# Kernel optimization log

Hardware: AMD Instinct MI355X
Metric: run time of the kernel (lower is better)

Reference implementation:

```python
import jax, jax.numpy as jnp
import numpy as np

D_MODEL = 2048
N_HEADS = 16
HEAD_DIM = 128
KV_RANK = 512


def setup_inputs() -> dict:
    key = jax.random.key(0)
    ks = jax.random.split(key, 6)
    s = lambda fan_in: 1.0 / np.sqrt(fan_in)
    return {
        "x": jax.random.normal(ks[0], (2, 2048, D_MODEL), dtype=jnp.float32),
        "Wq": jax.random.normal(ks[1], (D_MODEL, N_HEADS * HEAD_DIM), dtype=jnp.float32) * s(D_MODEL),
        "Wdown": jax.random.normal(ks[2], (D_MODEL, KV_RANK), dtype=jnp.float32) * s(D_MODEL),
        "Wk_up": jax.random.normal(ks[3], (KV_RANK, N_HEADS * HEAD_DIM), dtype=jnp.float32) * s(KV_RANK),
        "Wv_up": jax.random.normal(ks[4], (KV_RANK, N_HEADS * HEAD_DIM), dtype=jnp.float32) * s(KV_RANK),
        "Wo": jax.random.normal(ks[5], (N_HEADS * HEAD_DIM, D_MODEL), dtype=jnp.float32) * s(N_HEADS * HEAD_DIM),
    }


def reference(x, Wq, Wdown, Wk_up, Wv_up, Wo):
    B, T, _ = x.shape
    H, Dh = N_HEADS, HEAD_DIM
    # Q projection: (B,T,H,Dh) -> (B,H,T,Dh)
    Q = (x @ Wq).reshape(B, T, H, Dh).transpose(0, 2, 1, 3)
    # latent compression (this is the cached tensor)
    c = x @ Wdown  # (B, T, kv_lora_rank)
    # up-project latent to full K/V heads
    K = (c @ Wk_up).reshape(B, T, H, Dh).transpose(0, 2, 1, 3)
    V = (c @ Wv_up).reshape(B, T, H, Dh).transpose(0, 2, 1, 3)
    # causal SDPA (mask=None, past_kv=None -> is_causal=True), dropout=0
    scale = Dh ** (-0.5)
    scores = jnp.einsum("bhqd,bhkd->bhqk", Q, K) * scale
    causal = jnp.tril(jnp.ones((T, T), dtype=bool))
    scores = jnp.where(causal[None, None], scores, jnp.finfo(scores.dtype).min)
    attn = jax.nn.softmax(scores, axis=-1)
    out = jnp.einsum("bhqk,bhkd->bhqd", attn, V)
    out = out.transpose(0, 2, 1, 3).reshape(B, T, H * Dh)
    return out @ Wo, c
```

## Files before the change

### kernel.cpp

```cpp
#include <hip/hip_runtime.h>

typedef short bf16x8 __attribute__((ext_vector_type(8)));
typedef float f32x4 __attribute__((ext_vector_type(4)));

__device__ __forceinline__ void async16(const void* g, const void* l) {
  __builtin_amdgcn_global_load_lds(
      (const __attribute__((address_space(1))) unsigned int*)g,
      (__attribute__((address_space(3))) unsigned int*)(void*)(uintptr_t)l,
      16, 0, 0);
}

__device__ __forceinline__ unsigned short f2b(float f) {
  unsigned int u = __float_as_uint(f);
  u += 0x7fffu + ((u >> 16) & 1u);
  return (unsigned short)(u >> 16);
}

__global__ __launch_bounds__(256) void cast_f32_bf16(
    const float* __restrict__ in, unsigned short* __restrict__ out, int n) {
  int i = (blockIdx.x * 256 + threadIdx.x) * 4;
  if (i < n) {
    float4 v = *(const float4*)(in + i);
    ushort4 o;
    o.x = f2b(v.x); o.y = f2b(v.y); o.z = f2b(v.z); o.w = f2b(v.w);
    *(ushort4*)(out + i) = o;
  }
}

__global__ __launch_bounds__(256) void transpose_cast(
    const float* __restrict__ in, unsigned short* __restrict__ out,
    int K, int N) {
  __shared__ __align__(16) unsigned short tile[64][65];
  const int k0 = blockIdx.y * 64, n0 = blockIdx.x * 64;
  const int tid = threadIdx.x;
  const int r = tid >> 4, c4 = tid & 15;
#pragma unroll
  for (int p = 0; p < 4; ++p) {
    int row = p * 16 + r;
    float4 v = *(const float4*)(in + (size_t)(k0 + row) * N + n0 + c4 * 4);
    tile[c4 * 4 + 0][row] = f2b(v.x);
    tile[c4 * 4 + 1][row] = f2b(v.y);
    tile[c4 * 4 + 2][row] = f2b(v.z);
    tile[c4 * 4 + 3][row] = f2b(v.w);
  }
  __syncthreads();
#pragma unroll
  for (int p = 0; p < 4; ++p) {
    int nr = p * 16 + r;
    ushort4 o;
    o.x = tile[nr][c4 * 4 + 0];
    o.y = tile[nr][c4 * 4 + 1];
    o.z = tile[nr][c4 * 4 + 2];
    o.w = tile[nr][c4 * 4 + 3];
    *(ushort4*)(out + (size_t)(n0 + nr) * K + k0 + c4 * 4) = o;
  }
}

__global__ __launch_bounds__(256) void gemm_bt(
    const unsigned short* __restrict__ A, const unsigned short* __restrict__ BT,
    unsigned short* __restrict__ Cb, float* __restrict__ Cf, int M, int N, int K,
    float cscale) {
  __shared__ __align__(16) unsigned short sA[2][128 * 64];
  __shared__ __align__(16) unsigned short sB[2][128 * 64];
  const int tid = threadIdx.x;
  const int wave = tid >> 6, lane = tid & 63;
  const int quad = lane >> 4, cl = lane & 15;
  const int m0 = blockIdx.y * 128, n0 = blockIdx.x * 128;
  const int wm = (wave >> 1) * 64, wn = (wave & 1) * 64;
  (void)M;

  f32x4 acc[4][4] = {};

  const int lr = lane >> 3;
  const int lc = (lane & 7) ^ lr;
  const unsigned short* gA = A + (size_t)(m0 + wave * 32 + lr) * K + lc * 8;
  const unsigned short* gB = BT + (size_t)(n0 + wave * 32 + lr) * K + lc * 8;
  const int nk = K >> 6;

#pragma unroll
  for (int r = 0; r < 4; ++r) {
    async16(gA + (size_t)r * 8 * K, (char*)sA[0] + (wave * 32 + r * 8) * 128);
    async16(gB + (size_t)r * 8 * K, (char*)sB[0] + (wave * 32 + r * 8) * 128);
  }
  __syncthreads();

  for (int kt = 0; kt < nk; ++kt) {
    const int cur = kt & 1;
    if (kt + 1 < nk) {
      const int k1 = (kt + 1) * 64;
#pragma unroll
      for (int r = 0; r < 4; ++r) {
        async16(gA + (size_t)r * 8 * K + k1,
                (char*)sA[cur ^ 1] + (wave * 32 + r * 8) * 128);
        async16(gB + (size_t)r * 8 * K + k1,
                (char*)sB[cur ^ 1] + (wave * 32 + r * 8) * 128);
      }
    }
    const char* cA = (const char*)sA[cur];
    const char* cB = (const char*)sB[cur];
#pragma unroll
    for (int kk = 0; kk < 2; ++kk) {
      const int g = kk * 4 + quad;
      bf16x8 af[4], bfr[4];
#pragma unroll
      for (int i = 0; i < 4; ++i) {
        int row = wm + i * 16 + cl;
        af[i] = *(const bf16x8*)(cA + row * 128 + (g ^ (cl & 7)) * 16);
      }
#pragma unroll
      for (int j = 0; j < 4; ++j) {
        int row = wn + j * 16 + cl;
        bfr[j] = *(const bf16x8*)(cB + row * 128 + (g ^ (cl & 7)) * 16);
      }
#pragma unroll
      for (int i = 0; i < 4; ++i)
#pragma unroll
        for (int j = 0; j < 4; ++j)
          acc[i][j] = __builtin_amdgcn_mfma_f32_16x16x32_bf16(af[i], bfr[j], acc[i][j], 0, 0, 0);
    }
    __syncthreads();
  }
#pragma unroll
  for (int i = 0; i < 4; ++i)
#pragma unroll
    for (int j = 0; j < 4; ++j)
#pragma unroll
      for (int r = 0; r < 4; ++r) {
        int row = m0 + wm + i * 16 + quad * 4 + r;
        int col = n0 + wn + j * 16 + cl;
        float v = acc[i][j][r];
        if (Cb) Cb[(size_t)row * N + col] = f2b(v * cscale);
        if (Cf) Cf[(size_t)row * N + col] = v;
      }
}

__global__ __launch_bounds__(256) void gemm_qc(
    const unsigned short* __restrict__ A, const unsigned short* __restrict__ BT,
    unsigned short* __restrict__ Qb, unsigned short* __restrict__ cb,
    float* __restrict__ cout, int K, float qscale) {
  __shared__ __align__(16) unsigned short sA[2][128 * 64];
  __shared__ __align__(16) unsigned short sB[2][128 * 64];
  const int tid = threadIdx.x;
  const int wave = tid >> 6, lane = tid & 63;
  const int quad = lane >> 4, cl = lane & 15;
  const int m0 = blockIdx.y * 128, n0 = blockIdx.x * 128;
  const int wm = (wave >> 1) * 64, wn = (wave & 1) * 64;

  f32x4 acc[4][4] = {};

  const int lr = lane >> 3;
  const int lc = (lane & 7) ^ lr;
  const unsigned short* gA = A + (size_t)(m0 + wave * 32 + lr) * K + lc * 8;
  const unsigned short* gB = BT + (size_t)(n0 + wave * 32 + lr) * K + lc * 8;
  const int nk = K >> 6;

#pragma unroll
  for (int r = 0; r < 4; ++r) {
    async16(gA + (size_t)r * 8 * K, (char*)sA[0] + (wave * 32 + r * 8) * 128);
    async16(gB + (size_t)r * 8 * K, (char*)sB[0] + (wave * 32 + r * 8) * 128);
  }
  __syncthreads();

  for (int kt = 0; kt < nk; ++kt) {
    const int cur = kt & 1;
    if (kt + 1 < nk) {
      const int k1 = (kt + 1) * 64;
#pragma unroll
      for (int r = 0; r < 4; ++r) {
        async16(gA + (size_t)r * 8 * K + k1,
                (char*)sA[cur ^ 1] + (wave * 32 + r * 8) * 128);
        async16(gB + (size_t)r * 8 * K + k1,
                (char*)sB[cur ^ 1] + (wave * 32 + r * 8) * 128);
      }
    }
    const char* cA = (const char*)sA[cur];
    const char* cB = (const char*)sB[cur];
#pragma unroll
    for (int kk = 0; kk < 2; ++kk) {
      const int g = kk * 4 + quad;
      bf16x8 af[4], bfr[4];
#pragma unroll
      for (int i = 0; i < 4; ++i) {
        int row = wm + i * 16 + cl;
        af[i] = *(const bf16x8*)(cA + row * 128 + (g ^ (cl & 7)) * 16);
      }
#pragma unroll
      for (int j = 0; j < 4; ++j) {
        int row = wn + j * 16 + cl;
        bfr[j] = *(const bf16x8*)(cB + row * 128 + (g ^ (cl & 7)) * 16);
      }
#pragma unroll
      for (int i = 0; i < 4; ++i)
#pragma unroll
        for (int j = 0; j < 4; ++j)
          acc[i][j] = __builtin_amdgcn_mfma_f32_16x16x32_bf16(af[i], bfr[j], acc[i][j], 0, 0, 0);
    }
    __syncthreads();
  }
  const bool qreg = (n0 < 2048);
#pragma unroll
  for (int i = 0; i < 4; ++i)
#pragma unroll
    for (int j = 0; j < 4; ++j)
#pragma unroll
      for (int r = 0; r < 4; ++r) {
        int row = m0 + wm + i * 16 + quad * 4 + r;
        int col = n0 + wn + j * 16 + cl;
        float v = acc[i][j][r];
        if (qreg) {
          Qb[(size_t)row * 2048 + col] = f2b(v * qscale);
        } else {
          int c2 = col - 2048;
          cb[(size_t)row * 512 + c2] = f2b(v);
          cout[(size_t)row * 512 + c2] = v;
        }
      }
}

__global__ __launch_bounds__(256) void mla_attn(
    const unsigned short* __restrict__ Qm, const unsigned short* __restrict__ Km,
    const unsigned short* __restrict__ Vt, unsigned short* __restrict__ Om, int T) {
  const int ld = 2048;
  const int ldv = 4096;
  __shared__ __align__(16) unsigned short sK[2][64 * 128];
  __shared__ __align__(16) unsigned short sVT[128 * 64];
  __shared__ __align__(16) unsigned short sP[64 * 64];
  const int h = blockIdx.y, b = blockIdx.z;
  const int tid = threadIdx.x, wave = tid >> 6, lane = tid & 63;
  const int quad = lane >> 4, cl = lane & 15;
  const int nq = T / 64;

  for (int phase = 0; phase < 2; ++phase) {
    const int qt = phase ? (nq - 1 - blockIdx.x) : blockIdx.x;

    bf16x8 qf[4];
    {
      const unsigned short* Qg =
          Qm + (size_t)(b * T + qt * 64 + wave * 16 + cl) * ld + h * 128 + quad * 8;
#pragma unroll
      for (int kk = 0; kk < 4; ++kk)
        qf[kk] = *(const bf16x8*)(Qg + kk * 32);
    }

    float m_i[4], l_part[4];
    f32x4 acc_o[8] = {};
#pragma unroll
    for (int r = 0; r < 4; ++r) { m_i[r] = -1e30f; l_part[r] = 0.f; }

    const unsigned short* Kg0 = Km + (size_t)(b * T) * ld + h * 128;
    const unsigned short* Vg0 = Vt + (size_t)(h * 128) * ldv + (size_t)b * T;

#pragma unroll
    for (int r = 0; r < 4; ++r) {
      int c0 = r * 256 + wave * 64;
      int c = c0 + lane;
      int row = c >> 4, j = (c & 15) ^ (row & 7);
      async16(Kg0 + (size_t)row * ld + j * 8, (char*)sK[0] + c0 * 16);
    }
    __syncthreads();

    for (int kt = 0; kt <= qt; ++kt) {
      const int cur = kt & 1;
      const char* cK = (const char*)sK[cur];

      if (kt < qt) {
        const unsigned short* Kg = Kg0 + (size_t)(kt + 1) * 64 * ld;
        char* dK = (char*)sK[cur ^ 1];
#pragma unroll
        for (int r = 0; r < 4; ++r) {
          int c0 = r * 256 + wave * 64;
          int c = c0 + lane;
          int row = c >> 4, j = (c & 15) ^ (row & 7);
          async16(Kg + (size_t)row * ld + j * 8, dK + c0 * 16);
        }
      }
      {
        const unsigned short* Vg = Vg0 + kt * 64;
#pragma unroll
        for (int r = 0; r < 4; ++r) {
          int c0 = r * 256 + wave * 64;
          int c = c0 + lane;
          int d = c >> 3, jv = (c & 7) ^ (d & 7);
          async16(Vg + (size_t)d * ldv + jv * 8, (char*)sVT + c0 * 16);
        }
      }

      f32x4 s[4] = {};
      __builtin_amdgcn_s_setprio(1);
#pragma unroll
      for (int kk = 0; kk < 4; ++kk) {
#pragma unroll
        for (int j = 0; j < 4; ++j) {
          int t = j * 16 + cl;
          int jp = (kk * 4 + quad) ^ (t & 7);
          bf16x8 bk = *(const bf16x8*)(cK + (t * 16 + jp) * 16);
          s[j] = __builtin_amdgcn_mfma_f32_16x16x32_bf16(qf[kk], bk, s[j], 0, 0, 0);
        }
      }
      __builtin_amdgcn_s_setprio(0);

      const bool need_mask = (kt == qt);
#pragma unroll
      for (int r = 0; r < 4; ++r) {
        int q_l = wave * 16 + quad * 4 + r;
        float mxl = -1e30f;
#pragma unroll
        for (int j = 0; j < 4; ++j) {
          float v = s[j][r];
          if (need_mask) {
            int t_l = j * 16 + cl;
            if (t_l > q_l) v = -1e30f;
            s[j][r] = v;
          }
          mxl = fmaxf(mxl, v);
        }
        if (__any(mxl > m_i[r] + 6.f)) {
          float mx = mxl;
#pragma unroll
          for (int off = 1; off < 16; off <<= 1)
            mx = fmaxf(mx, __shfl_xor(mx, off));
          float m_new = fmaxf(m_i[r], mx);
          float alpha = exp2f(m_i[r] - m_new);
          m_i[r] = m_new;
          l_part[r] *= alpha;
#pragma unroll
          for (int jd = 0; jd < 8; ++jd)
            acc_o[jd][r] *= alpha;
        }
        float rs = 0.f;
#pragma unroll
        for (int j = 0; j < 4; ++j) {
          float p = exp2f(s[j][r] - m_i[r]);
          s[j][r] = p;
          rs += p;
        }
        l_part[r] += rs;
      }

#pragma unroll
      for (int j = 0; j < 4; ++j)
#pragma unroll
        for (int r = 0; r < 4; ++r) {
          int q = wave * 16 + quad * 4 + r;
          int swz = (q & 7) ^ (((q >> 3) & 1) << 1);
          int t = j * 16 + cl;
          int jp = (t >> 3) ^ swz;
          sP[(q * 8 + jp) * 8 + (t & 7)] = f2b(s[j][r]);
        }

      __syncthreads();

      __builtin_amdgcn_s_setprio(1);
#pragma unroll
      for (int kk2 = 0; kk2 < 2; ++kk2) {
        int q = wave * 16 + cl;
        int swz = (q & 7) ^ (((q >> 3) & 1) << 1);
        int jp = (kk2 * 4 + quad) ^ swz;
        bf16x8 ap = *(const bf16x8*)((const char*)sP + (q * 8 + jp) * 16);
#pragma unroll
        for (int jd = 0; jd < 8; ++jd) {
          int d = jd * 16 + cl;
          int jpv = (kk2 * 4 + quad) ^ (d & 7);
          bf16x8 bv = *(const bf16x8*)((const char*)sVT + (d * 8 + jpv) * 16);
          acc_o[jd] = __builtin_amdgcn_mfma_f32_16x16x32_bf16(ap, bv, acc_o[jd], 0, 0, 0);
        }
      }
      __builtin_amdgcn_s_setprio(0);

      __syncthreads();
    }

#pragma unroll
    for (int r = 0; r < 4; ++r) {
      float l = l_part[r];
#pragma unroll
      for (int off = 1; off < 16; off <<= 1)
        l += __shfl_xor(l, off);
      float inv = 1.f / l;
      int row = b * T + qt * 64 + wave * 16 + quad * 4 + r;
#pragma unroll
      for (int jd = 0; jd < 8; ++jd)
        Om[(size_t)row * ld + h * 128 + jd * 16 + cl] = f2b(acc_o[jd][r] * inv);
    }
  }
}

extern "C" void kernel_launch(void* const* d_in, const int* in_sizes, int n_in,
                              void* d_out, int out_size, void* d_ws, size_t ws_size,
                              hipStream_t stream) {
  (void)in_sizes; (void)n_in; (void)out_size; (void)ws_size;
  const int B = 2, T = 2048, Dm = 2048, H = 16, Dh = 128, R = 512;
  const int M = B * T;
  const float* x     = (const float*)d_in[0];
  const float* Wq    = (const float*)d_in[1];
  const float* Wdown = (const float*)d_in[2];
  const float* Wkup  = (const float*)d_in[3];
  const float* Wvup  = (const float*)d_in[4];
  const float* Wo    = (const float*)d_in[5];

  float* out  = (float*)d_out;
  float* cout = out + (size_t)M * Dm;

  unsigned short* ws  = (unsigned short*)d_ws;
  unsigned short* WqT = ws;
  unsigned short* WdT = WqT + (size_t)Dm * Dm;
  unsigned short* WoT = WdT + (size_t)R * Dm;
  unsigned short* WkT = WoT + (size_t)Dm * Dm;
  unsigned short* WvT = WkT + (size_t)Dm * R;
  unsigned short* xb  = WvT + (size_t)Dm * R;
  unsigned short* cb  = xb + (size_t)M * Dm;
  unsigned short* Qb  = cb + (size_t)M * R;
  unsigned short* Kb  = Qb + (size_t)M * Dm;
  unsigned short* VT  = Kb + (size_t)M * Dm;
  unsigned short* AO  = xb;

  const float qscale = 0.08838834764831845f * 1.4426950408889634f;

  cast_f32_bf16<<<(M * Dm) / 1024, 256, 0, stream>>>(x, xb, M * Dm);
  transpose_cast<<<dim3(32, 32), 256, 0, stream>>>(Wq, WqT, Dm, Dm);
  transpose_cast<<<dim3(8, 32), 256, 0, stream>>>(Wdown, WdT, Dm, R);
  transpose_cast<<<dim3(32, 32), 256, 0, stream>>>(Wo, WoT, Dm, Dm);
  transpose_cast<<<dim3(32, 8), 256, 0, stream>>>(Wkup, WkT, R, Dm);
  transpose_cast<<<dim3(32, 8), 256, 0, stream>>>(Wvup, WvT, R, Dm);

  gemm_qc<<<dim3(20, 32), 256, 0, stream>>>(xb, WqT, Qb, cb, cout, Dm, qscale);

  gemm_bt<<<dim3(Dm / 128, M / 128), 256, 0, stream>>>(cb, WkT, Kb, nullptr, M, Dm, R, 1.f);
  gemm_bt<<<dim3(M / 128, Dm / 128), 256, 0, stream>>>(WvT, cb, VT, nullptr, Dm, M, R, 1.f);

  mla_attn<<<dim3(T / 128, H, B), 256, 0, stream>>>(Qb, Kb, VT, AO, T);

  gemm_bt<<<dim3(Dm / 128, M / 128), 256, 0, stream>>>(AO, WoT, nullptr, out, M, Dm, Dm, 1.f);
  (void)Dh; (void)H;
}
```

Before: 368.2 us.

## Fuse K/V up-projection GEMMs and double-buffer V tiles in attention

Result: slower. 413.2 us (+12.2%).

```diff
diff --git a/kernel.cpp b/kernel.cpp
--- a/kernel.cpp
+++ b/kernel.cpp
@@ -217,21 +217,113 @@
       }
 }
 
+__global__ __launch_bounds__(256) void gemm_kv(
+    const unsigned short* __restrict__ cb, const unsigned short* __restrict__ WkT,
+    const unsigned short* __restrict__ WvT, unsigned short* __restrict__ Kb,
+    unsigned short* __restrict__ VT) {
+  __shared__ __align__(16) unsigned short sA[2][128 * 64];
+  __shared__ __align__(16) unsigned short sB[2][128 * 64];
+  const int tid = threadIdx.x;
+  const int wave = tid >> 6, lane = tid & 63;
+  const int quad = lane >> 4, cl = lane & 15;
+  const int wm = (wave >> 1) * 64, wn = (wave & 1) * 64;
+  const int K = 512;
+
+  const unsigned short *A, *BT;
+  unsigned short* C;
+  int N, m0, n0;
+  const int f = blockIdx.x;
+  if (f < 512) {
+    A = cb; BT = WkT; C = Kb; N = 2048;
+    m0 = (f >> 4) * 128; n0 = (f & 15) * 128;
+  } else {
+    const int g2 = f - 512;
+    A = WvT; BT = cb; C = VT; N = 4096;
+    m0 = (g2 >> 5) * 128; n0 = (g2 & 31) * 128;
+  }
+
+  f32x4 acc[4][4] = {};
+
+  const int lr = lane >> 3;
+  const int lc = (lane & 7) ^ lr;
+  const unsigned short* gA = A + (size_t)(m0 + wave * 32 + lr) * K + lc * 8;
+  const unsigned short* gB = BT + (size_t)(n0 + wave * 32 + lr) * K + lc * 8;
+  const int nk = K >> 6;
+
+#pragma unroll
+  for (int r = 0; r < 4; ++r) {
+    async16(gA + (size_t)r * 8 * K, (char*)sA[0] + (wave * 32 + r * 8) * 128);
+    async16(gB + (size_t)r * 8 * K, (char*)sB[0] + (wave * 32 + r * 8) * 128);
+  }
+  __syncthreads();
+
+  for (int kt = 0; kt < nk; ++kt) {
+    const int cur = kt & 1;
+    if (kt + 1 < nk) {
+      const int k1 = (kt + 1) * 64;
+#pragma unroll
+      for (int r = 0; r < 4; ++r) {
+        async16(gA + (size_t)r * 8 * K + k1,
+                (char*)sA[cur ^ 1] + (wave * 32 + r * 8) * 128);
+        async16(gB + (size_t)r * 8 * K + k1,
+                (char*)sB[cur ^ 1] + (wave * 32 + r * 8) * 128);
+      }
+    }
+    const char* cA = (const char*)sA[cur];
+    const char* cB = (const char*)sB[cur];
+#pragma unroll
+    for (int kk = 0; kk < 2; ++kk) {
+      const int g = kk * 4 + quad;
+      bf16x8 af[4], bfr[4];
+#pragma unroll
+      for (int i = 0; i < 4; ++i) {
+        int row = wm + i * 16 + cl;
+        af[i] = *(const bf16x8*)(cA + row * 128 + (g ^ (cl & 7)) * 16);
+      }
+#pragma unroll
+      for (int j = 0; j < 4; ++j) {
+        int row = wn + j * 16 + cl;
+        bfr[j] = *(const bf16x8*)(cB + row * 128 + (g ^ (cl & 7)) * 16);
+      }
+#pragma unroll
+      for (int i = 0; i < 4; ++i)
+#pragma unroll
+        for (int j = 0; j < 4; ++j)
+          acc[i][j] = __builtin_amdgcn_mfma_f32_16x16x32_bf16(af[i], bfr[j], acc[i][j], 0, 0, 0);
+    }
+    __syncthreads();
+  }
+#pragma unroll
+  for (int i = 0; i < 4; ++i)
+#pragma unroll
+    for (int j = 0; j < 4; ++j)
+#pragma unroll
+      for (int r = 0; r < 4; ++r) {
+        int row = m0 + wm + i * 16 + quad * 4 + r;
+        int col = n0 + wn + j * 16 + cl;
+        C[(size_t)row * N + col] = f2b(acc[i][j][r]);
+      }
+}
+
 __global__ __launch_bounds__(256) void mla_attn(
     const unsigned short* __restrict__ Qm, const unsigned short* __restrict__ Km,
     const unsigned short* __restrict__ Vt, unsigned short* __restrict__ Om, int T) {
   const int ld = 2048;
   const int ldv = 4096;
   __shared__ __align__(16) unsigned short sK[2][64 * 128];
-  __shared__ __align__(16) unsigned short sVT[128 * 64];
+  __shared__ __align__(16) unsigned short sVT[2][128 * 64];
   __shared__ __align__(16) unsigned short sP[64 * 64];
-  const int h = blockIdx.y, b = blockIdx.z;
+  const int f = blockIdx.x + 16 * blockIdx.y + 256 * blockIdx.z;
+  const int c8 = f & 7, jj = f >> 3;
+  const int g = c8 * 4 + (jj >> 4);
+  const int bxr = jj & 15;
+  const int h = g & 15, b = g >> 4;
   const int tid = threadIdx.x, wave = tid >> 6, lane = tid & 63;
   const int quad = lane >> 4, cl = lane & 15;
   const int nq = T / 64;
 
   for (int phase = 0; phase < 2; ++phase) {
-    const int qt = phase ? (nq - 1 - blockIdx.x) : blockIdx.x;
+    const int qt = phase ? (nq - 1 - bxr) : bxr;
 
     bf16x8 qf[4];
     {
@@ -250,18 +342,22 @@
     const unsigned short* Kg0 = Km + (size_t)(b * T) * ld + h * 128;
     const unsigned short* Vg0 = Vt + (size_t)(h * 128) * ldv + (size_t)b * T;
 
+    __syncthreads();
 #pragma unroll
     for (int r = 0; r < 4; ++r) {
       int c0 = r * 256 + wave * 64;
       int c = c0 + lane;
       int row = c >> 4, j = (c & 15) ^ (row & 7);
       async16(Kg0 + (size_t)row * ld + j * 8, (char*)sK[0] + c0 * 16);
+      int d = c >> 3, jv = (c & 7) ^ (d & 7);
+      async16(Vg0 + (size_t)d * ldv + jv * 8, (char*)sVT[0] + c0 * 16);
     }
     __syncthreads();
 
     for (int kt = 0; kt <= qt; ++kt) {
       const int cur = kt & 1;
       const char* cK = (const char*)sK[cur];
+      const char* cV = (const char*)sVT[cur];
 
       if (kt < qt) {
         const unsigned short* Kg = Kg0 + (size_t)(kt + 1) * 64 * ld;
@@ -274,19 +370,8 @@
           async16(Kg + (size_t)row * ld + j * 8, dK + c0 * 16);
         }
       }
-      {
-        const unsigned short* Vg = Vg0 + kt * 64;
-#pragma unroll
-        for (int r = 0; r < 4; ++r) {
-          int c0 = r * 256 + wave * 64;
-          int c = c0 + lane;
-          int d = c >> 3, jv = (c & 7) ^ (d & 7);
-          async16(Vg + (size_t)d * ldv + jv * 8, (char*)sVT + c0 * 16);
-        }
-      }
 
       f32x4 s[4] = {};
-      __builtin_amdgcn_s_setprio(1);
 #pragma unroll
       for (int kk = 0; kk < 4; ++kk) {
 #pragma unroll
@@ -297,7 +382,6 @@
           s[j] = __builtin_amdgcn_mfma_f32_16x16x32_bf16(qf[kk], bk, s[j], 0, 0, 0);
         }
       }
-      __builtin_amdgcn_s_setprio(0);
 
       const bool need_mask = (kt == qt);
 #pragma unroll
@@ -350,7 +434,18 @@
 
       __syncthreads();
 
-      __builtin_amdgcn_s_setprio(1);
+      if (kt < qt) {
+        const unsigned short* Vg = Vg0 + (kt + 1) * 64;
+        char* dV = (char*)sVT[cur ^ 1];
+#pragma unroll
+        for (int r = 0; r < 4; ++r) {
+          int c0 = r * 256 + wave * 64;
+          int c = c0 + lane;
+          int d = c >> 3, jv = (c & 7) ^ (d & 7);
+          async16(Vg + (size_t)d * ldv + jv * 8, dV + c0 * 16);
+        }
+      }
+
 #pragma unroll
       for (int kk2 = 0; kk2 < 2; ++kk2) {
         int q = wave * 16 + cl;
@@ -361,13 +456,10 @@
         for (int jd = 0; jd < 8; ++jd) {
           int d = jd * 16 + cl;
           int jpv = (kk2 * 4 + quad) ^ (d & 7);
-          bf16x8 bv = *(const bf16x8*)((const char*)sVT + (d * 8 + jpv) * 16);
+          bf16x8 bv = *(const bf16x8*)(cV + (d * 8 + jpv) * 16);
           acc_o[jd] = __builtin_amdgcn_mfma_f32_16x16x32_bf16(ap, bv, acc_o[jd], 0, 0, 0);
         }
       }
-      __builtin_amdgcn_s_setprio(0);
-
-      __syncthreads();
     }
 
 #pragma unroll
@@ -425,8 +517,7 @@
 
   gemm_qc<<<dim3(20, 32), 256, 0, stream>>>(xb, WqT, Qb, cb, cout, Dm, qscale);
 
-  gemm_bt<<<dim3(Dm / 128, M / 128), 256, 0, stream>>>(cb, WkT, Kb, nullptr, M, Dm, R, 1.f);
-  gemm_bt<<<dim3(M / 128, Dm / 128), 256, 0, stream>>>(WvT, cb, VT, nullptr, Dm, M, R, 1.f);
+  gemm_kv<<<1024, 256, 0, stream>>>(cb, WkT, WvT, Kb, VT);
 
   mla_attn<<<dim3(T / 128, H, B), 256, 0, stream>>>(Qb, Kb, VT, AO, T);
 
```
